# Kernel tuning notes

Hardware: AMD Instinct MI355X
Metric: run time of the kernel (lower is better)

The kernel has to match this reference:

```python
import jax, jax.numpy as jnp
import numpy as np

N, E, D, G, C = 50000, 800000, 128, 64, 2
SCALE = 1.0 / np.sqrt(D).astype(np.float32)


def setup_inputs() -> dict:
    key = jax.random.key(0)
    ks = jax.random.split(key, 32)
    inp = {
        "x": jax.random.normal(ks[0], (N, D), dtype=jnp.float32),
        "edge_index": jax.random.randint(ks[1], (2, E), 0, N),
        "batch": jnp.sort(jax.random.randint(ks[2], (N,), 0, G)),
    }
    i = 3
    for l in range(2):
        for nm in ("Wq", "Wk", "Wv", "Ws"):
            inp[f"{nm}{l}"] = jax.random.normal(ks[i], (D, D), dtype=jnp.float32) * 0.05
            i += 1
        for nm in ("bq", "bk", "bv", "bs"):
            inp[f"{nm}{l}"] = jnp.zeros((D,), dtype=jnp.float32)
    inp["Wc1"] = jax.random.normal(ks[i], (D // 2, D), dtype=jnp.float32) * 0.05
    inp["bc1"] = jnp.zeros((D // 2,), dtype=jnp.float32)
    inp["Wc2"] = jax.random.normal(ks[i + 1], (C, D // 2), dtype=jnp.float32) * 0.05
    inp["bc2"] = jnp.zeros((C,), dtype=jnp.float32)
    return inp


def _transformer_conv(x, src, dst, Wq, bq, Wk, bk, Wv, bv, Ws, bs):
    # PyG TransformerConv, heads=1, concat=True, root_weight=True, beta=False.
    q = x @ Wq.T + bq            # [N, D] node-level projections, then gather per edge
    k = x @ Wk.T + bk
    v = x @ Wv.T + bv
    alpha = jnp.sum(q[dst] * k[src], axis=-1) * SCALE          # [E]
    # segment softmax over incoming edges of each target node
    m = jax.ops.segment_max(alpha, dst, num_segments=N)         # [N]
    ea = jnp.exp(alpha - m[dst])
    denom = jax.ops.segment_sum(ea, dst, num_segments=N)        # [N]
    w = ea / denom[dst]                                         # [E]
    out = jax.ops.segment_sum(v[src] * w[:, None], dst, num_segments=N)  # [N, D]
    return out + x @ Ws.T + bs   # skip connection (lin_skip)


def reference(x, edge_index, batch,
              Wq0, bq0, Wk0, bk0, Wv0, bv0, Ws0, bs0,
              Wq1, bq1, Wk1, bk1, Wv1, bv1, Ws1, bs1,
              Wc1, bc1, Wc2, bc2):
    src, dst = edge_index[0], edge_index[1]
    h = _transformer_conv(x, src, dst, Wq0, bq0, Wk0, bk0, Wv0, bv0, Ws0, bs0)
    h = jax.nn.relu(h)  # dropout is a no-op in eval mode
    h = _transformer_conv(h, src, dst, Wq1, bq1, Wk1, bk1, Wv1, bv1, Ws1, bs1)
    h = jax.nn.relu(h)
    # global mean pool over graphs
    sums = jax.ops.segment_sum(h, batch, num_segments=G)        # [G, D]
    cnts = jax.ops.segment_sum(jnp.ones((h.shape[0],), h.dtype), batch, num_segments=G)
    pooled = sums / jnp.maximum(cnts, 1.0)[:, None]
    # classifier MLP: [D -> D//2 -> C]
    z = jax.nn.relu(pooled @ Wc1.T + bc1)
    return z @ Wc2.T + bc2
```

## Files before the change

kernel.cpp:

```cpp
#include <hip/hip_runtime.h>
#include <math.h>

typedef __bf16 bf16x8 __attribute__((ext_vector_type(8)));
typedef float  f32x4  __attribute__((ext_vector_type(4)));
typedef float  f32x2  __attribute__((ext_vector_type(2)));
typedef unsigned short ushort_t;
typedef unsigned short ushort8 __attribute__((ext_vector_type(8)));

constexpr int Nn = 50000;
constexpr int Ee = 800000;
constexpr int Dd = 128;
constexpr int Gg = 64;
constexpr float SCALE = 0.08838834764831845f;
constexpr float QS    = 16.0f;
constexpr float ISC   = SCALE / (QS * QS);

__device__ inline ushort_t f2bf(float f) {
    unsigned u = __float_as_uint(f);
    unsigned r = (u + 0x7FFF + ((u >> 16) & 1)) >> 16;
    return (ushort_t)r;
}
__device__ inline float bf2f(ushort_t b) { return __uint_as_float(((unsigned)b) << 16); }

__device__ inline char q_i8(float f) {
    int v = (int)rintf(f * QS);
    v = max(-127, min(127, v));
    return (char)v;
}

__device__ inline void fp8x4_to_f32(int w, float* out) {
    f32x2 lo = __builtin_amdgcn_cvt_pk_f32_fp8(w, false);
    f32x2 hi = __builtin_amdgcn_cvt_pk_f32_fp8(w, true);
    out[0] = lo[0]; out[1] = lo[1]; out[2] = hi[0]; out[3] = hi[1];
}


constexpr int EB  = (Ee + 255) / 256;
constexpr int NBD = (Nn + 255) / 256;
constexpr int CWB = 64;
constexpr int N4  = Nn * Dd / 4;
constexpr int CXB = N4 / 256;

__global__ __launch_bounds__(256) void prep_kernel(
    const int* __restrict__ dst, int* __restrict__ counts, int* __restrict__ rank,
    const int* __restrict__ batch, int* __restrict__ startg, int* __restrict__ endg,
    const float* w0, const float* w1, const float* w2, const float* w3,
    const float* w4, const float* w5, const float* w6, const float* w7,
    ushort_t* __restrict__ Wfh, ushort_t* __restrict__ Wfl,
    const float* __restrict__ x, ushort_t* __restrict__ Xh, ushort_t* __restrict__ Xl) {
    int b = blockIdx.x;
    if (b < EB) {
        int e = b * 256 + threadIdx.x;
        if (e < Ee) rank[e] = atomicAdd(&counts[dst[e]], 1);
    } else if (b < EB + NBD) {
        int n = (b - EB) * 256 + threadIdx.x;
        if (n >= Nn) return;
        int g = batch[n];
        if (n == Nn - 1 || batch[n + 1] != g) endg[g] = n + 1;
        if (n == 0 || batch[n - 1] != g) startg[g] = n;
    } else if (b < EB + NBD + CWB) {
        const float* ws[8] = {w0, w1, w2, w3, w4, w5, w6, w7};
        int b2 = b - (EB + NBD);
        int m = b2 >> 3;
        int tt = (b2 & 7) * 256 + threadIdx.x;
        int lane = tt & 63;
        int ln = lane & 15, quad = lane >> 4;
        int n = (tt >> 9) * 32 + ((tt >> 8) & 1) * 16 + ln;
        int k0 = ((tt >> 6) & 3) * 32 + quad * 8;
        const float* srcp = ws[m] + n * 128 + k0;
        float4 a = *(const float4*)(srcp);
        float4 bb = *(const float4*)(srcp + 4);
        float e[8] = {a.x, a.y, a.z, a.w, bb.x, bb.y, bb.z, bb.w};
        ushort8 h, l;
#pragma unroll
        for (int j = 0; j < 8; ++j) {
            h[j] = f2bf(e[j]);
            l[j] = f2bf(e[j] - bf2f(h[j]));
        }
        size_t o = (size_t)m * 16384 + (size_t)tt * 8;
        *(ushort8*)(Wfh + o) = h;
        *(ushort8*)(Wfl + o) = l;
    } else {
        int i = (b - (EB + NBD + CWB)) * 256 + threadIdx.x;
        if (i >= N4) return;
        float4 xv = ((const float4*)x)[i];
        ushort4 h, l;
        h.x = f2bf(xv.x); l.x = f2bf(xv.x - bf2f(h.x));
        h.y = f2bf(xv.y); l.y = f2bf(xv.y - bf2f(h.y));
        h.z = f2bf(xv.z); l.z = f2bf(xv.z - bf2f(h.z));
        h.w = f2bf(xv.w); l.w = f2bf(xv.w - bf2f(h.w));
        ((ushort4*)Xh)[i] = h;
        ((ushort4*)Xl)[i] = l;
    }
}


__global__ __launch_bounds__(256) void scan1_kernel(const int* __restrict__ counts,
                                                    int* __restrict__ offsets,
                                                    int* __restrict__ blockSums) {
    __shared__ int sh[256];
    int i = blockIdx.x * 256 + threadIdx.x;
    int v = (i < Nn) ? counts[i] : 0;
    sh[threadIdx.x] = v;
    __syncthreads();
    for (int off = 1; off < 256; off <<= 1) {
        int t = (threadIdx.x >= off) ? sh[threadIdx.x - off] : 0;
        __syncthreads();
        sh[threadIdx.x] += t;
        __syncthreads();
    }
    if (i < Nn) offsets[i] = sh[threadIdx.x] - v;
    if (threadIdx.x == 255) blockSums[blockIdx.x] = sh[255];
}

__global__ __launch_bounds__(256) void scan2_kernel(int* __restrict__ blockSums, int nb) {
    __shared__ int sh[256];
    int t = threadIdx.x;
    int v = (t < nb) ? blockSums[t] : 0;
    sh[t] = v;
    __syncthreads();
    for (int off = 1; off < 256; off <<= 1) {
        int u = (t >= off) ? sh[t - off] : 0;
        __syncthreads();
        sh[t] += u;
        __syncthreads();
    }
    if (t < nb) blockSums[t] = sh[t] - v;
}

__global__ __launch_bounds__(256) void scan3_kernel(int* __restrict__ offsets,
                                                    const int* __restrict__ blockSums) {
    int i = blockIdx.x * 256 + threadIdx.x;
    if (i < Nn) offsets[i] += blockSums[blockIdx.x];
    if (i == 0) offsets[Nn] = Ee;
}


constexpr int XS = 136;

__device__ __attribute__((always_inline)) void gemm_body(int bx, int which,
    const ushort_t* __restrict__ Xh, const ushort_t* __restrict__ Xl,
    const ushort_t* __restrict__ Wfh, const ushort_t* __restrict__ Wfl,
    int lw,
    const float* __restrict__ b0, const float* __restrict__ b1,
    const float* __restrict__ b2, const float* __restrict__ b3,
    char* __restrict__ Oq, char* __restrict__ Okv,
    ushort_t* __restrict__ Os) {
    __shared__ ushort_t XhS[64 * XS];
    __shared__ ushort_t XlS[64 * XS];
    const ushort_t* wfh = Wfh + (size_t)(lw + which) * 16384;
    const ushort_t* wfl = Wfl + (size_t)(lw + which) * 16384;
    const float* bias = (which == 0) ? b0 : (which == 1) ? b1 : (which == 2) ? b2 : b3;
    char* O8 = (which == 0) ? Oq : (which == 1) ? Okv : Okv + 128;
    int   o8str = (which == 0) ? 128 : 256;

    int w = threadIdx.x >> 6;
    int lane = threadIdx.x & 63;
    int quad = lane >> 4, ln = lane & 15;
    int n0 = w * 32;

    bf16x8 bh[2][4], bl[2][4];
#pragma unroll
    for (int ct = 0; ct < 2; ++ct)
#pragma unroll
        for (int kc = 0; kc < 4; ++kc) {
            int off = (w * 512 + ct * 256 + kc * 64 + lane) * 8;
            bh[ct][kc] = *(const bf16x8*)(wfh + off);
            bl[ct][kc] = *(const bf16x8*)(wfl + off);
        }
    float bias0 = bias[n0 + ln];
    float bias1 = bias[n0 + 16 + ln];

    int rowBase = bx * 256;
    int trow = threadIdx.x >> 4;
    int tcol = (threadIdx.x & 15) * 8;

    for (int chunk = 0; chunk < 4; ++chunk) {
        int cbase = rowBase + chunk * 64;
        __syncthreads();
#pragma unroll
        for (int rr = 0; rr < 4; ++rr) {
            int lrow = trow + rr * 16;
            int grow = min(cbase + lrow, Nn - 1);
            *(ushort8*)(&XhS[lrow * XS + tcol]) =
                *(const ushort8*)(Xh + (size_t)grow * 128 + tcol);
            *(ushort8*)(&XlS[lrow * XS + tcol]) =
                *(const ushort8*)(Xl + (size_t)grow * 128 + tcol);
        }
        __syncthreads();

#pragma unroll
        for (int rt = 0; rt < 4; ++rt) {
            const ushort_t* ph = &XhS[(rt * 16 + ln) * XS + quad * 8];
            const ushort_t* pl = &XlS[(rt * 16 + ln) * XS + quad * 8];
            bf16x8 ah[4], al[4];
#pragma unroll
            for (int kc = 0; kc < 4; ++kc) {
                ah[kc] = *(const bf16x8*)(ph + kc * 32);
                al[kc] = *(const bf16x8*)(pl + kc * 32);
            }
            f32x4 acc00 = {0.f,0.f,0.f,0.f}, acc01 = {0.f,0.f,0.f,0.f};
            f32x4 acc10 = {0.f,0.f,0.f,0.f}, acc11 = {0.f,0.f,0.f,0.f};
#pragma unroll
            for (int kc = 0; kc < 2; ++kc) {
                int k2 = kc + 2;
                acc00 = __builtin_amdgcn_mfma_f32_16x16x32_bf16(ah[kc], bh[0][kc], acc00, 0, 0, 0);
                acc01 = __builtin_amdgcn_mfma_f32_16x16x32_bf16(ah[kc], bh[1][kc], acc01, 0, 0, 0);
                acc10 = __builtin_amdgcn_mfma_f32_16x16x32_bf16(ah[k2], bh[0][k2], acc10, 0, 0, 0);
                acc11 = __builtin_amdgcn_mfma_f32_16x16x32_bf16(ah[k2], bh[1][k2], acc11, 0, 0, 0);
                acc00 = __builtin_amdgcn_mfma_f32_16x16x32_bf16(ah[kc], bl[0][kc], acc00, 0, 0, 0);
                acc01 = __builtin_amdgcn_mfma_f32_16x16x32_bf16(ah[kc], bl[1][kc], acc01, 0, 0, 0);
                acc10 = __builtin_amdgcn_mfma_f32_16x16x32_bf16(ah[k2], bl[0][k2], acc10, 0, 0, 0);
                acc11 = __builtin_amdgcn_mfma_f32_16x16x32_bf16(ah[k2], bl[1][k2], acc11, 0, 0, 0);
                acc00 = __builtin_amdgcn_mfma_f32_16x16x32_bf16(al[kc], bh[0][kc], acc00, 0, 0, 0);
                acc01 = __builtin_amdgcn_mfma_f32_16x16x32_bf16(al[kc], bh[1][kc], acc01, 0, 0, 0);
                acc10 = __builtin_amdgcn_mfma_f32_16x16x32_bf16(al[k2], bh[0][k2], acc10, 0, 0, 0);
                acc11 = __builtin_amdgcn_mfma_f32_16x16x32_bf16(al[k2], bh[1][k2], acc11, 0, 0, 0);
            }
            int m0 = cbase + rt * 16;
            int orow0 = m0 + quad * 4;
            bool full = (orow0 + 3) < Nn;
#pragma unroll
            for (int reg = 0; reg < 4; ++reg) {
                int orow = orow0 + reg;
                if (full || orow < Nn) {
                    float o0 = acc00[reg] + acc10[reg] + bias0;
                    float o1 = acc01[reg] + acc11[reg] + bias1;
                    if (which <= 1) {
                        size_t ob = (size_t)orow * o8str;
                        O8[ob + n0 + ln]      = q_i8(o0);
                        O8[ob + n0 + 16 + ln] = q_i8(o1);
                    } else if (which == 2) {
                        int pk = __builtin_amdgcn_cvt_pk_fp8_f32(o0, o1, 0, false);
                        size_t ob = (size_t)orow * 256;
                        O8[ob + n0 + ln]      = (char)(pk & 0xff);
                        O8[ob + n0 + 16 + ln] = (char)((pk >> 8) & 0xff);
                    } else {
                        size_t ob = (size_t)orow * 128;
                        Os[ob + n0 + ln]      = f2bf(o0);
                        Os[ob + n0 + 16 + ln] = f2bf(o1);
                    }
                }
            }
        }
    }
}

__global__ __launch_bounds__(256) void gemm_mfma_kernel(
    const ushort_t* __restrict__ Xh, const ushort_t* __restrict__ Xl,
    const ushort_t* __restrict__ Wfh, const ushort_t* __restrict__ Wfl,
    int lw,
    const float* __restrict__ b0, const float* __restrict__ b1,
    const float* __restrict__ b2, const float* __restrict__ b3,
    char* __restrict__ Oq, char* __restrict__ Okv,
    ushort_t* __restrict__ Os) {
    gemm_body(blockIdx.x, blockIdx.y, Xh, Xl, Wfh, Wfl, lw, b0, b1, b2, b3, Oq, Okv, Os);
}

constexpr int G0B = 196 * 4;

__global__ __launch_bounds__(256) void gemm0_scatter_kernel(
    const ushort_t* __restrict__ Xh, const ushort_t* __restrict__ Xl,
    const ushort_t* __restrict__ Wfh, const ushort_t* __restrict__ Wfl,
    const float* __restrict__ b0, const float* __restrict__ b1,
    const float* __restrict__ b2, const float* __restrict__ b3,
    char* __restrict__ Oq, char* __restrict__ Okv, ushort_t* __restrict__ Os,
    const int* __restrict__ src, const int* __restrict__ dst,
    const int* __restrict__ offsets, const int* __restrict__ rank,
    int* __restrict__ sorted_src) {
    int b = blockIdx.x;
    if (b >= G0B) {
        int e = (b - G0B) * 256 + threadIdx.x;
        if (e < Ee) sorted_src[offsets[dst[e]] + rank[e]] = src[e];
        return;
    }
    gemm_body(b % 196, b / 196, Xh, Xl, Wfh, Wfl, 0, b0, b1, b2, b3, Oq, Okv, Os);
}


__global__ __launch_bounds__(256) void attn_kernel(const char* __restrict__ q,
                                                   const char* __restrict__ kv,
                                                   const ushort_t* __restrict__ s,
                                                   const int* __restrict__ offsets,
                                                   const int* __restrict__ sorted_src,
                                                   ushort_t* __restrict__ oh,
                                                   ushort_t* __restrict__ ol,
                                                   int write_split) {
    int wid = blockIdx.x * 4 + (threadIdx.x >> 6);
    if (wid >= Nn) return;
    int lane = threadIdx.x & 63;
    int g = lane >> 3;
    int gl = lane & 7;
    int4 qw = *(const int4*)(q + (size_t)wid * 128 + gl * 16);
    int beg = offsets[wid], end = offsets[wid + 1];

    float l = 0.f;
    float acc[16];
#pragma unroll
    for (int j = 0; j < 16; ++j) acc[j] = 0.f;

    for (int e = beg + g; e < end; e += 8) {
        int sidx = sorted_src[e];
        const char* kvp = kv + (size_t)sidx * 256 + gl * 16;
        int4 kw = *(const int4*)(kvp);
        int4 vw = *(const int4*)(kvp + 128);
        int di = __builtin_amdgcn_sdot4(qw.x, kw.x, 0, false);
        di = __builtin_amdgcn_sdot4(qw.y, kw.y, di, false);
        di = __builtin_amdgcn_sdot4(qw.z, kw.z, di, false);
        di = __builtin_amdgcn_sdot4(qw.w, kw.w, di, false);
        di += __shfl_xor(di, 1, 64);
        di += __shfl_xor(di, 2, 64);
        di += __shfl_xor(di, 4, 64);
        float pw = __expf((float)di * ISC);
        l += pw;
        float vf[16];
        fp8x4_to_f32(vw.x, vf);      fp8x4_to_f32(vw.y, vf + 4);
        fp8x4_to_f32(vw.z, vf + 8);  fp8x4_to_f32(vw.w, vf + 12);
#pragma unroll
        for (int j = 0; j < 16; ++j) acc[j] += pw * vf[j];
    }

#pragma unroll
    for (int off = 8; off <= 32; off <<= 1) {
        l += __shfl_xor(l, off, 64);
#pragma unroll
        for (int j = 0; j < 16; ++j) acc[j] += __shfl_xor(acc[j], off, 64);
    }

    if (g == 0) {
        float inv = (l > 0.f) ? (1.0f / l) : 0.f;
        const ushort_t* sp = s + (size_t)wid * 128 + gl * 16;
        ushort8 sa = *(const ushort8*)(sp);
        ushort8 sb = *(const ushort8*)(sp + 8);
        float ov[16];
#pragma unroll
        for (int j = 0; j < 8; ++j) {
            ov[j]     = fmaxf(acc[j] * inv + bf2f(sa[j]), 0.f);
            ov[j + 8] = fmaxf(acc[j + 8] * inv + bf2f(sb[j]), 0.f);
        }
        if (write_split) {
            ushort8 h0, h1, l0, l1;
#pragma unroll
            for (int j = 0; j < 8; ++j) {
                h0[j] = f2bf(ov[j]);     l0[j] = f2bf(ov[j] - bf2f(h0[j]));
                h1[j] = f2bf(ov[j + 8]); l1[j] = f2bf(ov[j + 8] - bf2f(h1[j]));
            }
            ushort_t* op = oh + (size_t)wid * 128 + gl * 16;
            ushort_t* lp = ol + (size_t)wid * 128 + gl * 16;
            *(ushort8*)(op)     = h0;
            *(ushort8*)(op + 8) = h1;
            *(ushort8*)(lp)     = l0;
            *(ushort8*)(lp + 8) = l1;
        } else {
            ushort8 h0, h1;
#pragma unroll
            for (int j = 0; j < 8; ++j) { h0[j] = f2bf(ov[j]); h1[j] = f2bf(ov[j + 8]); }
            ushort_t* op = oh + (size_t)wid * 128 + gl * 16;
            *(ushort8*)(op)     = h0;
            *(ushort8*)(op + 8) = h1;
        }
    }
}


__global__ __launch_bounds__(256) void pool_kernel(const ushort_t* __restrict__ hb,
                                                   const int* __restrict__ batch,
                                                   float* __restrict__ pooled) {
    __shared__ float ps[4][128];
    int n0 = blockIdx.x * 256;
    int t = threadIdx.x;
    int lane32 = t & 31, rowgrp = t >> 5;
    for (int i = t; i < 512; i += 256) ((float*)ps)[i] = 0.f;
    __syncthreads();
    int gfirst = batch[min(n0, Nn - 1)];
    int d0 = lane32 * 4;
    float a0 = 0.f, a1 = 0.f, a2 = 0.f, a3 = 0.f;
    int curg = -1;
    for (int rr = 0; rr < 32; ++rr) {
        int n = n0 + rowgrp + rr * 8;
        if (n >= Nn) break;
        int g = batch[n];
        if (g != curg) {
            if (curg >= 0) {
                int slot = curg - gfirst;
                if (slot < 4) {
                    atomicAdd(&ps[slot][d0],     a0);
                    atomicAdd(&ps[slot][d0 + 1], a1);
                    atomicAdd(&ps[slot][d0 + 2], a2);
                    atomicAdd(&ps[slot][d0 + 3], a3);
                } else {
                    atomicAdd(&pooled[curg * Dd + d0],     a0);
                    atomicAdd(&pooled[curg * Dd + d0 + 1], a1);
                    atomicAdd(&pooled[curg * Dd + d0 + 2], a2);
                    atomicAdd(&pooled[curg * Dd + d0 + 3], a3);
                }
                a0 = a1 = a2 = a3 = 0.f;
            }
            curg = g;
        }
        ushort4 hv = *(const ushort4*)(hb + (size_t)n * 128 + d0);
        a0 += bf2f(hv.x); a1 += bf2f(hv.y); a2 += bf2f(hv.z); a3 += bf2f(hv.w);
    }
    if (curg >= 0) {
        int slot = curg - gfirst;
        if (slot < 4) {
            atomicAdd(&ps[slot][d0],     a0);
            atomicAdd(&ps[slot][d0 + 1], a1);
            atomicAdd(&ps[slot][d0 + 2], a2);
            atomicAdd(&ps[slot][d0 + 3], a3);
        } else {
            atomicAdd(&pooled[curg * Dd + d0],     a0);
            atomicAdd(&pooled[curg * Dd + d0 + 1], a1);
            atomicAdd(&pooled[curg * Dd + d0 + 2], a2);
            atomicAdd(&pooled[curg * Dd + d0 + 3], a3);
        }
    }
    __syncthreads();
    int glast = batch[min(n0 + 255, Nn - 1)];
    int nslots = min(glast - gfirst + 1, 4);
    for (int i = t; i < nslots * 128; i += 256) {
        int slot = i >> 7, d = i & 127;
        atomicAdd(&pooled[(gfirst + slot) * Dd + d], ps[slot][d]);
    }
}

__global__ __launch_bounds__(64) void mlp_kernel(const float* __restrict__ pooled,
                                                 const int* __restrict__ startg,
                                                 const int* __restrict__ endg,
                                                 const float* __restrict__ Wc1,
                                                 const float* __restrict__ bc1,
                                                 const float* __restrict__ Wc2,
                                                 const float* __restrict__ bc2,
                                                 float* __restrict__ out) {
    __shared__ float pm[128];
    __shared__ float hid[64];
    int g = blockIdx.x, t = threadIdx.x;
    float cnt = fmaxf((float)(endg[g] - startg[g]), 1.0f);
    float invc = 1.0f / cnt;
    pm[t]      = pooled[g * 128 + t] * invc;
    pm[t + 64] = pooled[g * 128 + 64 + t] * invc;
    __syncthreads();
    float acc = bc1[t];
    for (int i = 0; i < 128; ++i) acc += pm[i] * Wc1[t * 128 + i];
    hid[t] = fmaxf(acc, 0.f);
    __syncthreads();
    if (t < 2) {
        float a = bc2[t];
        for (int i = 0; i < 64; ++i) a += hid[i] * Wc2[t * 64 + i];
        out[g * 2 + t] = a;
    }
}


extern "C" void kernel_launch(void* const* d_in, const int* in_sizes, int n_in,
                              void* d_out, int out_size, void* d_ws, size_t ws_size,
                              hipStream_t stream) {
    const float* x   = (const float*)d_in[0];
    const int*   ei  = (const int*)d_in[1];
    const int* batch = (const int*)d_in[2];
    const float* W[2][4];
    const float* B[2][4];
    for (int l = 0; l < 2; ++l) {
        for (int j = 0; j < 4; ++j) W[l][j] = (const float*)d_in[3 + l * 8 + j];
        for (int j = 0; j < 4; ++j) B[l][j] = (const float*)d_in[3 + l * 8 + 4 + j];
    }
    const float* Wc1 = (const float*)d_in[19];
    const float* bc1 = (const float*)d_in[20];
    const float* Wc2 = (const float*)d_in[21];
    const float* bc2 = (const float*)d_in[22];
    float* out = (float*)d_out;

    const int* src = ei;
    const int* dst = ei + Ee;

    char* p = (char*)d_ws;
    auto alloc = [&](size_t bytes) {
        void* r = (void*)p;
        p += (bytes + 255) & ~(size_t)255;
        return r;
    };
    char*     q  = (char*)alloc((size_t)Nn * 128);
    char*     kv = (char*)alloc((size_t)Nn * 256);
    ushort_t* ss = (ushort_t*)alloc((size_t)Nn * 128 * 2);
    ushort_t* hb = (ushort_t*)alloc((size_t)Nn * 128 * 2);
    ushort_t* Xh = (ushort_t*)alloc((size_t)Nn * 128 * 2);
    ushort_t* Xl = (ushort_t*)alloc((size_t)Nn * 128 * 2);
    ushort_t* Wfh = (ushort_t*)alloc((size_t)8 * 16384 * 2);
    ushort_t* Wfl = (ushort_t*)alloc((size_t)8 * 16384 * 2);
    char* zbase = p;
    int*   counts = (int*)alloc(Nn * 4);
    int*   startg = (int*)alloc(Gg * 4);
    int*   endg   = (int*)alloc(Gg * 4);
    float* pooled = (float*)alloc(Gg * Dd * 4);
    size_t zbytes = (size_t)(p - zbase);
    int* offsets    = (int*)alloc((size_t)(Nn + 1) * 4);
    int* rank       = (int*)alloc((size_t)Ee * 4);
    int* blockSums  = (int*)alloc(256 * 4);
    int* sorted_src = (int*)alloc((size_t)Ee * 4);

    hipMemsetAsync(zbase, 0, zbytes, stream);

    constexpr int NB = (Nn + 255) / 256;

    prep_kernel<<<EB + NBD + CWB + CXB, 256, 0, stream>>>(
        dst, counts, rank, batch, startg, endg,
        W[0][0], W[0][1], W[0][2], W[0][3], W[1][0], W[1][1], W[1][2], W[1][3],
        Wfh, Wfl, x, Xh, Xl);
    scan1_kernel<<<NB, 256, 0, stream>>>(counts, offsets, blockSums);
    scan2_kernel<<<1, 256, 0, stream>>>(blockSums, NB);
    scan3_kernel<<<NB, 256, 0, stream>>>(offsets, blockSums);

    gemm0_scatter_kernel<<<G0B + EB, 256, 0, stream>>>(
        Xh, Xl, Wfh, Wfl, B[0][0], B[0][1], B[0][2], B[0][3],
        q, kv, ss, src, dst, offsets, rank, sorted_src);

    attn_kernel<<<(Nn + 3) / 4, 256, 0, stream>>>(q, kv, ss, offsets, sorted_src,
                                                  Xh, Xl, 1);
    dim3 ggrid(196, 4);
    gemm_mfma_kernel<<<ggrid, 256, 0, stream>>>(Xh, Xl, Wfh, Wfl, 4,
                                                B[1][0], B[1][1], B[1][2], B[1][3],
                                                q, kv, ss);
    attn_kernel<<<(Nn + 3) / 4, 256, 0, stream>>>(q, kv, ss, offsets, sorted_src,
                                                  hb, hb, 0);

    pool_kernel<<<(Nn + 255) / 256, 256, 0, stream>>>(hb, batch, pooled);
    mlp_kernel<<<Gg, 64, 0, stream>>>(pooled, startg, endg, Wc1, bc1, Wc2, bc2, out);
}
```

Before: 327.6 us.

## Software-pipeline edge gathers and merge attention partials through shared memory

The attention kernel now prefetches the next edge's K/V row and the following source index one step ahead, so gather latency overlaps the dot-product and accumulation. Accumulation uses packed two-wide float vectors fed directly from the fp8 conversions. The final cross-group reduction moves from 48 xor-shuffles per lane to a shared-memory merge in which every lane sums two output columns and writes them, so all 64 lanes share the epilogue instead of only 8. This adds 16KB of LDS per block and extra registers for the prefetch, which may lower occupancy, and the merge relies on wave-level ordering with only a waitcnt and no barrier.

```diff
diff --git a/kernel.cpp b/kernel.cpp
--- a/kernel.cpp
+++ b/kernel.cpp
@@ -26,12 +26,6 @@
     int v = (int)rintf(f * QS);
     v = max(-127, min(127, v));
     return (char)v;
-}
-
-__device__ inline void fp8x4_to_f32(int w, float* out) {
-    f32x2 lo = __builtin_amdgcn_cvt_pk_f32_fp8(w, false);
-    f32x2 hi = __builtin_amdgcn_cvt_pk_f32_fp8(w, true);
-    out[0] = lo[0]; out[1] = lo[1]; out[2] = hi[0]; out[3] = hi[1];
 }
 
 
@@ -286,7 +280,9 @@
                                                    ushort_t* __restrict__ oh,
                                                    ushort_t* __restrict__ ol,
                                                    int write_split) {
-    int wid = blockIdx.x * 4 + (threadIdx.x >> 6);
+    __shared__ float merge[4][8][128];
+    int warp = threadIdx.x >> 6;
+    int wid = blockIdx.x * 4 + warp;
     if (wid >= Nn) return;
     int lane = threadIdx.x & 63;
     int g = lane >> 3;
@@ -295,15 +291,24 @@
     int beg = offsets[wid], end = offsets[wid + 1];
 
     float l = 0.f;
-    float acc[16];
-#pragma unroll
-    for (int j = 0; j < 16; ++j) acc[j] = 0.f;
-
-    for (int e = beg + g; e < end; e += 8) {
-        int sidx = sorted_src[e];
-        const char* kvp = kv + (size_t)sidx * 256 + gl * 16;
-        int4 kw = *(const int4*)(kvp);
-        int4 vw = *(const int4*)(kvp + 128);
+    f32x4 accq[4];
+#pragma unroll
+    for (int j = 0; j < 4; ++j) accq[j] = (f32x4){0.f, 0.f, 0.f, 0.f};
+    f32x2* acc = (f32x2*)accq;
+
+    int e = beg + g;
+    int s0 = (e < end) ? sorted_src[e] : 0;
+    int s1 = (e + 8 < end) ? sorted_src[e + 8] : 0;
+    const char* kvp0 = kv + (size_t)s0 * 256 + gl * 16;
+    int4 kw = *(const int4*)(kvp0);
+    int4 vw = *(const int4*)(kvp0 + 128);
+
+    for (; e < end; e += 8) {
+        const char* kvp1 = kv + (size_t)s1 * 256 + gl * 16;
+        int4 kw1 = *(const int4*)(kvp1);
+        int4 vw1 = *(const int4*)(kvp1 + 128);
+        int s2 = (e + 16 < end) ? sorted_src[e + 16] : 0;
+
         int di = __builtin_amdgcn_sdot4(qw.x, kw.x, 0, false);
         di = __builtin_amdgcn_sdot4(qw.y, kw.y, di, false);
         di = __builtin_amdgcn_sdot4(qw.z, kw.z, di, false);
@@ -313,52 +318,55 @@
         di += __shfl_xor(di, 4, 64);
         float pw = __expf((float)di * ISC);
         l += pw;
-        float vf[16];
-        fp8x4_to_f32(vw.x, vf);      fp8x4_to_f32(vw.y, vf + 4);
-        fp8x4_to_f32(vw.z, vf + 8);  fp8x4_to_f32(vw.w, vf + 12);
-#pragma unroll
-        for (int j = 0; j < 16; ++j) acc[j] += pw * vf[j];
-    }
-
-#pragma unroll
-    for (int off = 8; off <= 32; off <<= 1) {
-        l += __shfl_xor(l, off, 64);
-#pragma unroll
-        for (int j = 0; j < 16; ++j) acc[j] += __shfl_xor(acc[j], off, 64);
-    }
-
-    if (g == 0) {
-        float inv = (l > 0.f) ? (1.0f / l) : 0.f;
-        const ushort_t* sp = s + (size_t)wid * 128 + gl * 16;
-        ushort8 sa = *(const ushort8*)(sp);
-        ushort8 sb = *(const ushort8*)(sp + 8);
-        float ov[16];
-#pragma unroll
-        for (int j = 0; j < 8; ++j) {
-            ov[j]     = fmaxf(acc[j] * inv + bf2f(sa[j]), 0.f);
-            ov[j + 8] = fmaxf(acc[j + 8] * inv + bf2f(sb[j]), 0.f);
-        }
-        if (write_split) {
-            ushort8 h0, h1, l0, l1;
-#pragma unroll
-            for (int j = 0; j < 8; ++j) {
-                h0[j] = f2bf(ov[j]);     l0[j] = f2bf(ov[j] - bf2f(h0[j]));
-                h1[j] = f2bf(ov[j + 8]); l1[j] = f2bf(ov[j + 8] - bf2f(h1[j]));
-            }
-            ushort_t* op = oh + (size_t)wid * 128 + gl * 16;
-            ushort_t* lp = ol + (size_t)wid * 128 + gl * 16;
-            *(ushort8*)(op)     = h0;
-            *(ushort8*)(op + 8) = h1;
-            *(ushort8*)(lp)     = l0;
-            *(ushort8*)(lp + 8) = l1;
-        } else {
-            ushort8 h0, h1;
-#pragma unroll
-            for (int j = 0; j < 8; ++j) { h0[j] = f2bf(ov[j]); h1[j] = f2bf(ov[j + 8]); }
-            ushort_t* op = oh + (size_t)wid * 128 + gl * 16;
-            *(ushort8*)(op)     = h0;
-            *(ushort8*)(op + 8) = h1;
-        }
+        f32x2 pw2 = {pw, pw};
+        {
+            f32x2 lo, hi;
+            lo = __builtin_amdgcn_cvt_pk_f32_fp8(vw.x, false);
+            hi = __builtin_amdgcn_cvt_pk_f32_fp8(vw.x, true);
+            acc[0] += pw2 * lo; acc[1] += pw2 * hi;
+            lo = __builtin_amdgcn_cvt_pk_f32_fp8(vw.y, false);
+            hi = __builtin_amdgcn_cvt_pk_f32_fp8(vw.y, true);
+            acc[2] += pw2 * lo; acc[3] += pw2 * hi;
+            lo = __builtin_amdgcn_cvt_pk_f32_fp8(vw.z, false);
+            hi = __builtin_amdgcn_cvt_pk_f32_fp8(vw.z, true);
+            acc[4] += pw2 * lo; acc[5] += pw2 * hi;
+            lo = __builtin_amdgcn_cvt_pk_f32_fp8(vw.w, false);
+            hi = __builtin_amdgcn_cvt_pk_f32_fp8(vw.w, true);
+            acc[6] += pw2 * lo; acc[7] += pw2 * hi;
+        }
+        kw = kw1; vw = vw1; s1 = s2;
+    }
+
+    float* mrow = &merge[warp][g][gl * 16];
+    *(f32x4*)(mrow + 0)  = accq[0];
+    *(f32x4*)(mrow + 4)  = accq[1];
+    *(f32x4*)(mrow + 8)  = accq[2];
+    *(f32x4*)(mrow + 12) = accq[3];
+    __builtin_amdgcn_sched_barrier(0);
+    asm volatile("s_waitcnt lgkmcnt(0)" ::: "memory");
+    __builtin_amdgcn_sched_barrier(0);
+
+    l += __shfl_xor(l, 8, 64);
+    l += __shfl_xor(l, 16, 64);
+    l += __shfl_xor(l, 32, 64);
+
+    int d0 = lane << 1;
+    f32x2 sum = {0.f, 0.f};
+#pragma unroll
+    for (int gg = 0; gg < 8; ++gg) sum += *(f32x2*)(&merge[warp][gg][d0]);
+
+    float inv = (l > 0.f) ? (1.0f / l) : 0.f;
+    ushort2 sv = *(const ushort2*)(s + (size_t)wid * 128 + d0);
+    float o0 = fmaxf(sum.x * inv + bf2f(sv.x), 0.f);
+    float o1 = fmaxf(sum.y * inv + bf2f(sv.y), 0.f);
+    ushort2 h;
+    h.x = f2bf(o0); h.y = f2bf(o1);
+    *(ushort2*)(oh + (size_t)wid * 128 + d0) = h;
+    if (write_split) {
+        ushort2 lo2;
+        lo2.x = f2bf(o0 - bf2f(h.x));
+        lo2.y = f2bf(o1 - bf2f(h.y));
+        *(ushort2*)(ol + (size_t)wid * 128 + d0) = lo2;
     }
 }
 
```

New measurement: 314.3 us. 4.1% less time.
